# Performance work log

Measured on AMD Instinct MI355X. Metric: run time of the kernel, lower is better.

Reference implementation:

```python
import jax, jax.numpy as jnp
import numpy as np

B, Q, DIM, HEADS, RPE_H, HGRID, WGRID, STRIDE = 2, 900, 256, 8, 512, 64, 64, 16
KV = HGRID * WGRID


def setup_inputs() -> dict:
    key = jax.random.key(0)
    ks = jax.random.split(key, 16)
    s = 0.02
    return {
        "hidden_states": jax.random.normal(ks[0], (B, Q, DIM), jnp.float32),
        "reference_points": jax.random.uniform(ks[1], (B, Q, 1, 4), jnp.float32),
        "key_value_states": jax.random.normal(ks[2], (B, KV, DIM), jnp.float32),
        "spatial_shapes": jnp.array([[HGRID, WGRID]], dtype=jnp.int64),
        "attention_mask": jax.random.randint(ks[3], (B, KV), 0, 2, jnp.int32),
        "mlp1_w1": jax.random.normal(ks[4], (RPE_H, 2), jnp.float32) * s,
        "mlp1_b1": jnp.zeros((RPE_H,), jnp.float32),
        "mlp1_w2": jax.random.normal(ks[5], (HEADS, RPE_H), jnp.float32) * s,
        "mlp2_w1": jax.random.normal(ks[6], (RPE_H, 2), jnp.float32) * s,
        "mlp2_b1": jnp.zeros((RPE_H,), jnp.float32),
        "mlp2_w2": jax.random.normal(ks[7], (HEADS, RPE_H), jnp.float32) * s,
        "q_w": jax.random.normal(ks[8], (DIM, DIM), jnp.float32) * s,
        "q_b": jnp.zeros((DIM,), jnp.float32),
        "k_w": jax.random.normal(ks[9], (DIM, DIM), jnp.float32) * s,
        "k_b": jnp.zeros((DIM,), jnp.float32),
        "v_w": jax.random.normal(ks[10], (DIM, DIM), jnp.float32) * s,
        "v_b": jnp.zeros((DIM,), jnp.float32),
        "o_w": jax.random.normal(ks[11], (DIM, DIM), jnp.float32) * s,
        "o_b": jnp.zeros((DIM,), jnp.float32),
    }


def _attn(hidden_states, reference_points, key_value_states, h, w, attention_mask,
          mlp1_w1, mlp1_b1, mlp1_w2, mlp2_w1, mlp2_b1, mlp2_w2,
          q_w, q_b, k_w, k_b, v_w, v_b, o_w, o_b):
    b, q_len, dim = hidden_states.shape
    nh = mlp1_w2.shape[0]
    hd = dim // nh
    scale = hd ** -0.5
    stride = STRIDE

    # boxes cxcywh -> x1y1x2y2, scaled to absolute pixel coords (reparam=False)
    c, sz = reference_points[..., :2], reference_points[..., 2:]
    ref = jnp.concatenate([c - sz / 2, c + sz / 2], axis=-1)  # (B,Q,1,4)
    mult = jnp.array([w * stride, h * stride, w * stride, h * stride], dtype=ref.dtype)
    ref = ref * mult

    pos_x = (jnp.arange(w, dtype=jnp.float32) + 0.5) * stride
    pos_y = (jnp.arange(h, dtype=jnp.float32) + 0.5) * stride
    dx = ref[..., 0::2] - pos_x[None, None, :, None]  # (B,Q,W,2)
    dy = ref[..., 1::2] - pos_y[None, None, :, None]  # (B,Q,H,2)

    # small MLPs: 2 -> rpe_hidden -> num_heads
    rpe_x = jax.nn.relu(dx @ mlp1_w1.T + mlp1_b1) @ mlp1_w2.T  # (B,Q,W,nh)
    rpe_y = jax.nn.relu(dy @ mlp2_w1.T + mlp2_b1) @ mlp2_w2.T  # (B,Q,H,nh)
    rpe = rpe_x[:, :, None, :, :] + rpe_y[:, :, :, None, :]    # (B,Q,H,W,nh)
    rpe = rpe.reshape(b, q_len, h * w, nh).transpose(0, 3, 1, 2)  # (B,nh,Q,K)

    queries = (hidden_states @ q_w.T + q_b).reshape(b, q_len, nh, hd).transpose(0, 2, 1, 3) * scale
    kv_len = key_value_states.shape[1]
    keys = (key_value_states @ k_w.T + k_b).reshape(b, kv_len, nh, hd).transpose(0, 2, 1, 3)
    values = (key_value_states @ v_w.T + v_b).reshape(b, kv_len, nh, hd).transpose(0, 2, 1, 3)

    scores = jnp.einsum('bhqd,bhkd->bhqk', queries, keys) + rpe
    scores = scores + attention_mask.astype(scores.dtype)[:, None, None] * (-100.0)
    probs = jax.nn.softmax(scores, axis=-1)
    ctx = jnp.einsum('bhqk,bhkd->bhqd', probs, values)
    ctx = ctx.transpose(0, 2, 1, 3).reshape(b, q_len, dim)
    return ctx @ o_w.T + o_b


def reference(hidden_states, reference_points, key_value_states, spatial_shapes, attention_mask,
              mlp1_w1, mlp1_b1, mlp1_w2, mlp2_w1, mlp2_b1, mlp2_w2,
              q_w, q_b, k_w, k_b, v_w, v_b, o_w, o_b):
    h = int(spatial_shapes[0, 0])
    w = int(spatial_shapes[0, 1])
    return _attn(hidden_states, reference_points, key_value_states, h, w, attention_mask,
                 mlp1_w1, mlp1_b1, mlp1_w2, mlp2_w1, mlp2_b1, mlp2_w2,
                 q_w, q_b, k_w, k_b, v_w, v_b, o_w, o_b)
```

## Files before the change

### kernel.cpp

```cpp
#include <hip/hip_runtime.h>
#include <math.h>

#define NB    2
#define NQ    900
#define NQP   960
#define NKV   4096
#define DIMM  256
#define NHEAD 8
#define HD    32
#define RPEH  512
#define GRID  64
#define SPLIT 4

#define LOG2E 1.4426950408889634f

typedef short short8 __attribute__((ext_vector_type(8)));
typedef float f32x4 __attribute__((ext_vector_type(4)));
typedef unsigned uint2v __attribute__((ext_vector_type(2)));
typedef unsigned short u16;
typedef unsigned short u16x4 __attribute__((ext_vector_type(4)));

__device__ inline u16 f2bf(float f) {
    unsigned u = __builtin_bit_cast(unsigned, f);
    u += 0x7fff + ((u >> 16) & 1);
    return (u16)(u >> 16);
}
__device__ inline unsigned cvtpk_bf16(float a, float b) {
    unsigned r;
    asm("v_cvt_pk_bf16_f32 %0, %1, %2" : "=v"(r) : "v"(a), "v"(b));
    return r;
}

#define HS4  115200
#define KV4  524288
#define W4   16384
__global__ __launch_bounds__(256) void conv_bf16(
    const float* __restrict__ hs, const float* __restrict__ kv,
    const float* __restrict__ qw, const float* __restrict__ kw,
    const float* __restrict__ vw,
    u16* __restrict__ hsbf, u16* __restrict__ kvbf,
    u16* __restrict__ qwbf, u16* __restrict__ kwbf, u16* __restrict__ vwbf)
{
    const int total = HS4 + KV4 + 3 * W4;
    for (int g = blockIdx.x * 256 + threadIdx.x; g < total; g += gridDim.x * 256) {
        const float* s; u16* d; int off;
        if (g < HS4)                       { s = hs; d = hsbf; off = g; }
        else if (g < HS4 + KV4)            { s = kv; d = kvbf; off = g - HS4; }
        else if (g < HS4 + KV4 + W4)       { s = qw; d = qwbf; off = g - HS4 - KV4; }
        else if (g < HS4 + KV4 + 2 * W4)   { s = kw; d = kwbf; off = g - HS4 - KV4 - W4; }
        else                               { s = vw; d = vwbf; off = g - HS4 - KV4 - 2 * W4; }
        f32x4 v = *(const f32x4*)(s + (size_t)off * 4);
        *(u16x4*)(d + (size_t)off * 4) =
            (u16x4){f2bf(v[0]), f2bf(v[1]), f2bf(v[2]), f2bf(v[3])};
    }
}

__global__ __launch_bounds__(256) void proj_mfma(
    const u16* __restrict__ A,
    const u16* __restrict__ W0, const float* __restrict__ B0,
    const u16* __restrict__ W1, const float* __restrict__ B1,
    u16* __restrict__ outRow, u16* __restrict__ outVt,
    int M, float scale)
{
    __shared__ u16 Abuf[2][4096];
    __shared__ u16 Bbuf[2][4096];

    const u16* W = W0; const float* bias = B0; bool vt = false;
    if (blockIdx.z == 1) { W = W1; bias = B1; vt = true; }

    const int t    = threadIdx.x;
    const int lane = t & 63;
    const int w    = t >> 6;
    const int wm   = w >> 1, wn = w & 1;
    const int m0   = blockIdx.x * 128;
    const int n0   = blockIdx.y * 128;

    const int r0 = t >> 2, c0 = t & 3;
    const int r1 = r0 + 64;
    const int s0 = r0 * 4 + (c0 ^ (r0 & 3));
    const int s1 = r1 * 4 + (c0 ^ (r1 & 3));
    const u16* Arow0 = A + (size_t)(m0 + r0) * DIMM + c0 * 8;
    const u16* Arow1 = A + (size_t)(m0 + r1) * DIMM + c0 * 8;
    const u16* Wrow0 = W + (size_t)(n0 + r0) * DIMM + c0 * 8;
    const u16* Wrow1 = W + (size_t)(n0 + r1) * DIMM + c0 * 8;

    const int fr = lane & 15, fkc = lane >> 4;
    int aslot[4], bslot[4];
    #pragma unroll
    for (int f = 0; f < 4; ++f) {
        int ar = wm * 64 + f * 16 + fr;
        int br = wn * 64 + f * 16 + fr;
        aslot[f] = ar * 4 + (fkc ^ (ar & 3));
        bslot[f] = br * 4 + (fkc ^ (br & 3));
    }
    float bv[4];
    #pragma unroll
    for (int f = 0; f < 4; ++f) bv[f] = bias[n0 + wn * 64 + f * 16 + fr];

    f32x4 acc[4][4] = {};

    {
        short8 a0 = *(const short8*)(Arow0);
        short8 a1 = *(const short8*)(Arow1);
        short8 b0 = *(const short8*)(Wrow0);
        short8 b1 = *(const short8*)(Wrow1);
        *(short8*)&Abuf[0][s0 * 8] = a0;
        *(short8*)&Abuf[0][s1 * 8] = a1;
        *(short8*)&Bbuf[0][s0 * 8] = b0;
        *(short8*)&Bbuf[0][s1 * 8] = b1;
    }
    __syncthreads();

    int cur = 0;
    for (int kt = 0; kt < 8; ++kt) {
        short8 na0, na1, nb0, nb1;
        if (kt < 7) {
            int ko = (kt + 1) * 32;
            na0 = *(const short8*)(Arow0 + ko);
            na1 = *(const short8*)(Arow1 + ko);
            nb0 = *(const short8*)(Wrow0 + ko);
            nb1 = *(const short8*)(Wrow1 + ko);
        }
        short8 af[4], bf[4];
        #pragma unroll
        for (int f = 0; f < 4; ++f) {
            af[f] = *(const short8*)&Abuf[cur][aslot[f] * 8];
            bf[f] = *(const short8*)&Bbuf[cur][bslot[f] * 8];
        }
        #pragma unroll
        for (int i = 0; i < 4; ++i)
            #pragma unroll
            for (int j = 0; j < 4; ++j)
                acc[i][j] = __builtin_amdgcn_mfma_f32_16x16x32_bf16(af[i], bf[j], acc[i][j], 0, 0, 0);
        if (kt < 7) {
            *(short8*)&Abuf[cur ^ 1][s0 * 8] = na0;
            *(short8*)&Abuf[cur ^ 1][s1 * 8] = na1;
            *(short8*)&Bbuf[cur ^ 1][s0 * 8] = nb0;
            *(short8*)&Bbuf[cur ^ 1][s1 * 8] = nb1;
        }
        __syncthreads();
        cur ^= 1;
    }

    #pragma unroll
    for (int i = 0; i < 4; ++i) {
        int mbase = m0 + wm * 64 + i * 16 + 4 * fkc;
        #pragma unroll
        for (int j = 0; j < 4; ++j) {
            int n = n0 + wn * 64 + j * 16 + fr;
            #pragma unroll
            for (int r = 0; r < 4; ++r) {
                int gm = mbase + r;
                if (gm < M) {
                    float v = (acc[i][j][r] + bv[j]) * scale;
                    if (!vt) {
                        outRow[(size_t)gm * DIMM + n] = f2bf(v);
                    } else {
                        int bb = gm >> 12, kvi = gm & 4095;
                        int hh = n >> 5, dd = n & 31;
                        outVt[(size_t)((bb * NHEAD + hh) * HD + dd) * NKV + kvi] = f2bf(v);
                    }
                }
            }
        }
    }
}

__global__ __launch_bounds__(256) void rpe_kernel(
    const float* __restrict__ ref_pts,
    const float* __restrict__ w1x, const float* __restrict__ b1x,
    const float* __restrict__ w2x,
    const float* __restrict__ w1y, const float* __restrict__ b1y,
    const float* __restrict__ w2y,
    float* __restrict__ rpex, float* __restrict__ rpey)
{
    __shared__ f32x4 wpk[RPEH];
    __shared__ float w2t[RPEH][NHEAD];
    __shared__ float2 red[3][4][4][64];

    const int t   = threadIdx.x;
    const int m   = blockIdx.x & 1;
    const int bq0 = (blockIdx.x >> 1) * 4;

    const float* w1 = m ? w1y : w1x;
    const float* b1 = m ? b1y : b1x;
    const float* w2 = m ? w2y : w2x;
    for (int r = t; r < RPEH; r += 256) {
        float a = w1[r * 2], b = w1[r * 2 + 1];
        wpk[r] = (f32x4){a, b, b1[r], a + b};
    }
    for (int i = t; i < RPEH * NHEAD; i += 256) {
        int h = i >> 9, r = i & 511;
        w2t[r][h] = w2[h * RPEH + r] * LOG2E;
    }
    __syncthreads();

    const int lane = t & 63;
    const int wv   = t >> 6;
    const float p  = (lane + 0.5f) * 16.f;

    float lo[4], hi[4];
    #pragma unroll
    for (int j = 0; j < 4; ++j) {
        const float* q = ref_pts + (size_t)(bq0 + j) * 4;
        float c = m ? q[1] : q[0];
        float s = m ? q[3] : q[2];
        lo[j] = (c - s * 0.5f) * 1024.f;
        hi[j] = (c + s * 0.5f) * 1024.f;
    }

    float2 acc[4][4] = {};
    const int r0 = wv * 128;
    #pragma unroll 4
    for (int rr = 0; rr < 128; ++rr) {
        int r = r0 + rr;
        f32x4 W  = wpk[r];
        f32x4 u0 = *(const f32x4*)&w2t[r][0];
        f32x4 u1 = *(const f32x4*)&w2t[r][4];
        float bp = W[3] * p;
        #pragma unroll
        for (int tk = 0; tk < 4; ++tk) {
            float al  = W[0] * lo[tk] + W[1] * hi[tk] + W[2];
            float hid = fmaxf(al - bp, 0.f);
            acc[tk][0].x += u0[0] * hid;  acc[tk][0].y += u0[1] * hid;
            acc[tk][1].x += u0[2] * hid;  acc[tk][1].y += u0[3] * hid;
            acc[tk][2].x += u1[0] * hid;  acc[tk][2].y += u1[1] * hid;
            acc[tk][3].x += u1[2] * hid;  acc[tk][3].y += u1[3] * hid;
        }
    }

    if (wv > 0) {
        #pragma unroll
        for (int tk = 0; tk < 4; ++tk)
            #pragma unroll
            for (int j = 0; j < 4; ++j)
                red[wv - 1][tk][j][lane] = acc[tk][j];
    }
    __syncthreads();
    if (wv == 0) {
        float* outp = m ? rpey : rpex;
        #pragma unroll
        for (int tk = 0; tk < 4; ++tk) {
            size_t base = (size_t)(bq0 + tk) * (NHEAD * GRID) + lane;
            #pragma unroll
            for (int j = 0; j < 4; ++j) {
                float2 s0 = red[0][tk][j][lane];
                float2 s1 = red[1][tk][j][lane];
                float2 s2 = red[2][tk][j][lane];
                float sx = acc[tk][j].x + s0.x + s1.x + s2.x;
                float sy = acc[tk][j].y + s0.y + s1.y + s2.y;
                outp[base + (2 * j) * GRID]     = sx;
                outp[base + (2 * j + 1) * GRID] = sy;
            }
        }
    }
}

__global__ __launch_bounds__(256) void attn_mfma(
    const u16* __restrict__ Qbf, const u16* __restrict__ Kbf,
    const u16* __restrict__ Vt,
    const float* __restrict__ RX, const float* __restrict__ RY,
    const int* __restrict__ mask,
    float* __restrict__ pctx, float2* __restrict__ pml)
{
    constexpr int KSEG = NKV / SPLIT;
    constexpr int NTS  = KSEG / 64;
    __shared__ short8 kbuf[2][4][64];
    __shared__ short8 vbuf[2][4][64];
    __shared__ unsigned pbuf[4][64][4];
    __shared__ float ry_s[NTS][68];
    __shared__ float mbuf[2][64];

    const int tid  = threadIdx.x;
    const int lane = tid & 63;
    const int w    = tid >> 6;
    const int q15  = lane & 15;
    const int g    = lane >> 4;
    const int qt = blockIdx.x, h = blockIdx.y;
    const int b  = blockIdx.z / SPLIT;
    const int sp = blockIdx.z % SPLIT;
    const int q0 = qt * 64;
    const int wq = w * 16 + q15;
    const int gq = q0 + wq;
    const bool qok = gq < NQ;
    const int kv0g = sp * KSEG;

    float rxr[16];
    {
        const float* rxrow = RX + (size_t)(b * NQ + (qok ? gq : 0)) * (NHEAD * GRID) + h * GRID;
        #pragma unroll
        for (int kt = 0; kt < 4; ++kt)
            #pragma unroll
            for (int r = 0; r < 4; ++r)
                rxr[kt * 4 + r] = qok ? rxrow[16 * kt + 4 * g + r] : 0.f;
    }
    for (int idx = tid; idx < NTS * 64; idx += 256) {
        int y = idx & (NTS - 1), q = idx / NTS;
        int gq2 = q0 + q;
        ry_s[y][q] = (gq2 < NQ)
            ? RY[(size_t)(b * NQ + gq2) * (NHEAD * GRID) + h * GRID + sp * NTS + y] : 0.f;
    }

    short8 qf = *(const short8*)(Qbf + ((size_t)(b * NQ + gq)) * DIMM + h * HD + 8 * g);

    const int sr = tid >> 2, sc = tid & 3;
    const int vd = tid >> 3, vc = tid & 7;
    const size_t kbase = ((size_t)(b * NKV + kv0g + sr)) * DIMM + h * HD + 8 * sc;
    const size_t vbase = ((size_t)((b * NHEAD + h) * HD + vd)) * NKV + kv0g + 8 * vc;

    kbuf[0][sr >> 4][(sr & 15) + 16 * sc] = *(const short8*)(Kbf + kbase);
    vbuf[0][(vc >> 2) * 2 + (vd >> 4)][16 * (vc & 3) + (vd & 15)] = *(const short8*)(Vt + vbase);
    if (tid < 64) mbuf[0][tid] = -(100.f * LOG2E) * (float)mask[b * NKV + kv0g + tid];
    __syncthreads();

    f32x4 cacc0 = {0.f, 0.f, 0.f, 0.f};
    f32x4 cacc1 = {0.f, 0.f, 0.f, 0.f};
    float m_run = -1e30f, l_run = 0.f;
    int cur = 0;

    for (int t = 0; t < NTS; ++t) {
        short8 rk = {}, rv = {};
        float rm = 0.f;
        if (t < NTS - 1) {
            size_t kvn = (size_t)(t + 1) * 64;
            rk = *(const short8*)(Kbf + kbase + kvn * DIMM);
            rv = *(const short8*)(Vt + vbase + kvn);
            if (tid < 64) rm = -(100.f * LOG2E) * (float)mask[b * NKV + kv0g + kvn + tid];
        }

        f32x4 zero = {0.f, 0.f, 0.f, 0.f};
        f32x4 s[4];
        __builtin_amdgcn_s_setprio(1);
        #pragma unroll
        for (int kt = 0; kt < 4; ++kt)
            s[kt] = __builtin_amdgcn_mfma_f32_16x16x32_bf16(kbuf[cur][kt][lane], qf, zero, 0, 0, 0);
        __builtin_amdgcn_s_setprio(0);

        float ryb = ry_s[t][wq];
        #pragma unroll
        for (int kt = 0; kt < 4; ++kt) {
            #pragma unroll
            for (int r = 0; r < 4; ++r)
                s[kt][r] += rxr[kt * 4 + r] + ryb + mbuf[cur][16 * kt + 4 * g + r];
        }

        float mk[4];
        #pragma unroll
        for (int kt = 0; kt < 4; ++kt)
            mk[kt] = fmaxf(fmaxf(s[kt][0], s[kt][1]), fmaxf(s[kt][2], s[kt][3]));
        float mloc = fmaxf(fmaxf(mk[0], mk[1]), fmaxf(mk[2], mk[3]));
        mloc = fmaxf(mloc, __shfl_xor(mloc, 16));
        mloc = fmaxf(mloc, __shfl_xor(mloc, 32));

        if (!__all(mloc <= m_run + 8.f)) {
            float mnew = fmaxf(m_run, mloc);
            float fsc  = exp2f(m_run - mnew);
            l_run *= fsc;
            cacc0 *= fsc;
            cacc1 *= fsc;
            m_run = mnew;
        }

        float psum = 0.f;
        #pragma unroll
        for (int kt = 0; kt < 4; ++kt)
            #pragma unroll
            for (int r = 0; r < 4; ++r) {
                float pv = exp2f(s[kt][r] - m_run);
                s[kt][r] = pv;
                psum += pv;
            }
        psum += __shfl_xor(psum, 16);
        psum += __shfl_xor(psum, 32);
        l_run += psum;

        __builtin_amdgcn_s_setprio(1);
        #pragma unroll
        for (int sk = 0; sk < 2; ++sk) {
            #pragma unroll
            for (int kk = 0; kk < 2; ++kk) {
                int kt = sk * 2 + kk;
                unsigned d0 = cvtpk_bf16(s[kt][0], s[kt][1]);
                unsigned d1 = cvtpk_bf16(s[kt][2], s[kt][3]);
                int lt = 16 * ((2 * kt + (g >> 1)) & 3) + q15;
                uint2v* dst = (uint2v*)&pbuf[w][lt][2 * (g & 1)];
                *dst = (uint2v){d0, d1};
            }
            short8 pf = *(const short8*)&pbuf[w][lane][0];
            cacc0 = __builtin_amdgcn_mfma_f32_16x16x32_bf16(vbuf[cur][sk * 2 + 0][lane], pf, cacc0, 0, 0, 0);
            cacc1 = __builtin_amdgcn_mfma_f32_16x16x32_bf16(vbuf[cur][sk * 2 + 1][lane], pf, cacc1, 0, 0, 0);
        }
        __builtin_amdgcn_s_setprio(0);

        if (t < NTS - 1) {
            kbuf[cur ^ 1][sr >> 4][(sr & 15) + 16 * sc] = rk;
            vbuf[cur ^ 1][(vc >> 2) * 2 + (vd >> 4)][16 * (vc & 3) + (vd & 15)] = rv;
            if (tid < 64) mbuf[cur ^ 1][tid] = rm;
        }
        __syncthreads();
        cur ^= 1;
    }

    size_t prow = (size_t)(sp * NB + b) * NQP + gq;
    float* pc = pctx + prow * DIMM + h * HD;
    #pragma unroll
    for (int r = 0; r < 4; ++r) {
        pc[4 * g + r]      = cacc0[r];
        pc[16 + 4 * g + r] = cacc1[r];
    }
    if (g == 0) {
        float2 v; v.x = m_run; v.y = l_run;
        pml[prow * NHEAD + h] = v;
    }
}

__global__ __launch_bounds__(256) void attn_reduce(
    const float* __restrict__ pctx, const float2* __restrict__ pml,
    float* __restrict__ CTX)
{
    const int bq = blockIdx.x;
    const int b = bq / NQ, q = bq - b * NQ;
    const int c = threadIdx.x;
    const int h = c >> 5;

    float m[SPLIT], l[SPLIT];
    #pragma unroll
    for (int sp = 0; sp < SPLIT; ++sp) {
        float2 v = pml[((size_t)(sp * NB + b) * NQP + q) * NHEAD + h];
        m[sp] = v.x; l[sp] = v.y;
    }
    float ms = fmaxf(fmaxf(m[0], m[1]), fmaxf(m[2], m[3]));
    float L = 0.f, acc = 0.f;
    #pragma unroll
    for (int sp = 0; sp < SPLIT; ++sp) {
        float wgt = exp2f(m[sp] - ms);
        L   += wgt * l[sp];
        acc += wgt * pctx[((size_t)(sp * NB + b) * NQP + q) * DIMM + c];
    }
    CTX[(size_t)bq * DIMM + c] = acc / L;
}

__global__ __launch_bounds__(256) void gemm_bias_f32(
    const float* __restrict__ A, const float* __restrict__ W,
    const float* __restrict__ bias, float* __restrict__ C,
    int M, int N, int K)
{
    __shared__ float As[32][33];
    __shared__ float Ws[32][33];
    const int t  = threadIdx.x;
    const int tr = t >> 4;
    const int tc = t & 15;
    const int brow = blockIdx.y * 32;
    const int bcol = blockIdx.x * 32;
    float acc00 = 0.f, acc01 = 0.f, acc10 = 0.f, acc11 = 0.f;

    for (int kt = 0; kt < K; kt += 32) {
        #pragma unroll
        for (int i = 0; i < 4; ++i) {
            int idx = t + i * 256;
            int r = idx >> 5, c = idx & 31;
            int gr = brow + r;
            As[r][c] = (gr < M) ? A[(size_t)gr * K + kt + c] : 0.f;
            Ws[r][c] = W[(size_t)(bcol + r) * K + kt + c];
        }
        __syncthreads();
        #pragma unroll 8
        for (int k = 0; k < 32; ++k) {
            float a0 = As[tr * 2][k], a1 = As[tr * 2 + 1][k];
            float w0 = Ws[tc * 2][k], w1 = Ws[tc * 2 + 1][k];
            acc00 += a0 * w0; acc01 += a0 * w1;
            acc10 += a1 * w0; acc11 += a1 * w1;
        }
        __syncthreads();
    }
    int gc0 = bcol + tc * 2, gc1 = gc0 + 1;
    int gr0 = brow + tr * 2, gr1 = gr0 + 1;
    if (gr0 < M) {
        C[(size_t)gr0 * N + gc0] = acc00 + bias[gc0];
        C[(size_t)gr0 * N + gc1] = acc01 + bias[gc1];
    }
    if (gr1 < M) {
        C[(size_t)gr1 * N + gc0] = acc10 + bias[gc0];
        C[(size_t)gr1 * N + gc1] = acc11 + bias[gc1];
    }
}

extern "C" void kernel_launch(void* const* d_in, const int* in_sizes, int n_in,
                              void* d_out, int out_size, void* d_ws, size_t ws_size,
                              hipStream_t stream)
{
    const float* hs   = (const float*)d_in[0];
    const float* rp   = (const float*)d_in[1];
    const float* kv   = (const float*)d_in[2];
    const int*   msk  = (const int*)d_in[4];
    const float* m1w1 = (const float*)d_in[5];
    const float* m1b1 = (const float*)d_in[6];
    const float* m1w2 = (const float*)d_in[7];
    const float* m2w1 = (const float*)d_in[8];
    const float* m2b1 = (const float*)d_in[9];
    const float* m2w2 = (const float*)d_in[10];
    const float* q_w  = (const float*)d_in[11];
    const float* q_b  = (const float*)d_in[12];
    const float* k_w  = (const float*)d_in[13];
    const float* k_b  = (const float*)d_in[14];
    const float* v_w  = (const float*)d_in[15];
    const float* v_b  = (const float*)d_in[16];
    const float* o_w  = (const float*)d_in[17];
    const float* o_b  = (const float*)d_in[18];
    float* out = (float*)d_out;

    char* p = (char*)d_ws;
    float* RX   = (float*)p; p += (size_t)NB * NQ * NHEAD * GRID * 4;
    float* RY   = (float*)p; p += (size_t)NB * NQ * NHEAD * GRID * 4;
    float* CTX  = (float*)p; p += (size_t)NB * NQ * DIMM * 4;
    u16*   Qbf  = (u16*)p;   p += (size_t)1920 * DIMM * 2;
    u16*   Kbf  = (u16*)p;   p += (size_t)NB * NKV * DIMM * 2;
    u16*   Vt   = (u16*)p;   p += (size_t)NB * NHEAD * HD * NKV * 2;

    char* u = p;
    u16* hsbf = (u16*)u;
    u16* kvbf = hsbf + (size_t)1920 * DIMM;
    u16* qwbf = kvbf + (size_t)NB * NKV * DIMM;
    u16* kwbf = qwbf + (size_t)DIMM * DIMM;
    u16* vwbf = kwbf + (size_t)DIMM * DIMM;
    float*  pctx = (float*)u;
    float2* pml  = (float2*)(pctx + (size_t)SPLIT * NB * NQP * DIMM);

    const float scale = 0.17677669529663687f * LOG2E;

    conv_bf16<<<1024, 256, 0, stream>>>(hs, kv, q_w, k_w, v_w,
                                        hsbf, kvbf, qwbf, kwbf, vwbf);

    proj_mfma<<<dim3(15, 2, 1), 256, 0, stream>>>(
        hsbf, qwbf, q_b, nullptr, nullptr, Qbf, nullptr, NB * NQ, scale);

    proj_mfma<<<dim3(64, 2, 2), 256, 0, stream>>>(
        kvbf, kwbf, k_b, vwbf, v_b, Kbf, Vt, NB * NKV, 1.f);

    rpe_kernel<<<900, 256, 0, stream>>>(rp, m1w1, m1b1, m1w2,
                                        m2w1, m2b1, m2w2, RX, RY);

    attn_mfma<<<dim3((NQ + 63) / 64, NHEAD, NB * SPLIT), 256, 0, stream>>>(
        Qbf, Kbf, Vt, RX, RY, msk, pctx, pml);

    attn_reduce<<<NB * NQ, 256, 0, stream>>>(pctx, pml, CTX);

    gemm_bias_f32<<<dim3(DIMM / 32, (NB * NQ + 31) / 32), 256, 0, stream>>>(
        CTX, o_w, o_b, out, NB * NQ, DIMM, DIMM);
}
```

Before: 141.6 us.

## Load K/V fragments directly from global memory, drop LDS staging and barriers

Removes the shared-memory double buffers for K, V, mask and RY in the attention kernel. Each wave now loads its MFMA operand fragments straight from global memory (relying on L1/L2 reuse across the four waves), which eliminates the per-tile __syncthreads. The mask is pre-converted to scaled floats in the conversion kernel so the attention loop can read it as vectors. The trade-off is four times more global/L2 traffic per block and no explicit prefetch, so global latency is exposed unless the compiler or other waves hide it.

```diff
diff --git a/kernel.cpp b/kernel.cpp
--- a/kernel.cpp
+++ b/kernel.cpp
@@ -17,6 +17,7 @@
 typedef short short8 __attribute__((ext_vector_type(8)));
 typedef float f32x4 __attribute__((ext_vector_type(4)));
 typedef unsigned uint2v __attribute__((ext_vector_type(2)));
+typedef int int4v __attribute__((ext_vector_type(4)));
 typedef unsigned short u16;
 typedef unsigned short u16x4 __attribute__((ext_vector_type(4)));
 
@@ -34,15 +35,25 @@
 #define HS4  115200
 #define KV4  524288
 #define W4   16384
+#define M4   2048
 __global__ __launch_bounds__(256) void conv_bf16(
     const float* __restrict__ hs, const float* __restrict__ kv,
     const float* __restrict__ qw, const float* __restrict__ kw,
-    const float* __restrict__ vw,
+    const float* __restrict__ vw, const int* __restrict__ msk,
     u16* __restrict__ hsbf, u16* __restrict__ kvbf,
-    u16* __restrict__ qwbf, u16* __restrict__ kwbf, u16* __restrict__ vwbf)
-{
-    const int total = HS4 + KV4 + 3 * W4;
+    u16* __restrict__ qwbf, u16* __restrict__ kwbf, u16* __restrict__ vwbf,
+    float* __restrict__ Mb)
+{
+    const int total = HS4 + KV4 + 3 * W4 + M4;
     for (int g = blockIdx.x * 256 + threadIdx.x; g < total; g += gridDim.x * 256) {
+        if (g >= HS4 + KV4 + 3 * W4) {
+            int off = g - (HS4 + KV4 + 3 * W4);
+            int4v m = *(const int4v*)(msk + (size_t)off * 4);
+            f32x4 o = {-(100.f * LOG2E) * (float)m[0], -(100.f * LOG2E) * (float)m[1],
+                       -(100.f * LOG2E) * (float)m[2], -(100.f * LOG2E) * (float)m[3]};
+            *(f32x4*)(Mb + (size_t)off * 4) = o;
+            continue;
+        }
         const float* s; u16* d; int off;
         if (g < HS4)                       { s = hs; d = hsbf; off = g; }
         else if (g < HS4 + KV4)            { s = kv; d = kvbf; off = g - HS4; }
@@ -260,16 +271,12 @@
     const u16* __restrict__ Qbf, const u16* __restrict__ Kbf,
     const u16* __restrict__ Vt,
     const float* __restrict__ RX, const float* __restrict__ RY,
-    const int* __restrict__ mask,
+    const float* __restrict__ Mb,
     float* __restrict__ pctx, float2* __restrict__ pml)
 {
     constexpr int KSEG = NKV / SPLIT;
     constexpr int NTS  = KSEG / 64;
-    __shared__ short8 kbuf[2][4][64];
-    __shared__ short8 vbuf[2][4][64];
     __shared__ unsigned pbuf[4][64][4];
-    __shared__ float ry_s[NTS][68];
-    __shared__ float mbuf[2][64];
 
     const int tid  = threadIdx.x;
     const int lane = tid & 63;
@@ -294,54 +301,47 @@
             for (int r = 0; r < 4; ++r)
                 rxr[kt * 4 + r] = qok ? rxrow[16 * kt + 4 * g + r] : 0.f;
     }
-    for (int idx = tid; idx < NTS * 64; idx += 256) {
-        int y = idx & (NTS - 1), q = idx / NTS;
-        int gq2 = q0 + q;
-        ry_s[y][q] = (gq2 < NQ)
-            ? RY[(size_t)(b * NQ + gq2) * (NHEAD * GRID) + h * GRID + sp * NTS + y] : 0.f;
-    }
+    const float* yrow = RY + (size_t)(b * NQ + (qok ? gq : 0)) * (NHEAD * GRID) + h * GRID + sp * NTS;
 
     short8 qf = *(const short8*)(Qbf + ((size_t)(b * NQ + gq)) * DIMM + h * HD + 8 * g);
 
-    const int sr = tid >> 2, sc = tid & 3;
-    const int vd = tid >> 3, vc = tid & 7;
-    const size_t kbase = ((size_t)(b * NKV + kv0g + sr)) * DIMM + h * HD + 8 * sc;
-    const size_t vbase = ((size_t)((b * NHEAD + h) * HD + vd)) * NKV + kv0g + 8 * vc;
-
-    kbuf[0][sr >> 4][(sr & 15) + 16 * sc] = *(const short8*)(Kbf + kbase);
-    vbuf[0][(vc >> 2) * 2 + (vd >> 4)][16 * (vc & 3) + (vd & 15)] = *(const short8*)(Vt + vbase);
-    if (tid < 64) mbuf[0][tid] = -(100.f * LOG2E) * (float)mask[b * NKV + kv0g + tid];
-    __syncthreads();
+    const u16* kb = Kbf + ((size_t)(b * NKV + kv0g + q15)) * DIMM + h * HD + 8 * g;
+    const u16* vb = Vt + ((size_t)((b * NHEAD + h) * HD + q15)) * NKV + kv0g + 8 * g;
+    const float* mb = Mb + (size_t)b * NKV + kv0g + 4 * g;
 
     f32x4 cacc0 = {0.f, 0.f, 0.f, 0.f};
     f32x4 cacc1 = {0.f, 0.f, 0.f, 0.f};
     float m_run = -1e30f, l_run = 0.f;
-    int cur = 0;
 
     for (int t = 0; t < NTS; ++t) {
-        short8 rk = {}, rv = {};
-        float rm = 0.f;
-        if (t < NTS - 1) {
-            size_t kvn = (size_t)(t + 1) * 64;
-            rk = *(const short8*)(Kbf + kbase + kvn * DIMM);
-            rv = *(const short8*)(Vt + vbase + kvn);
-            if (tid < 64) rm = -(100.f * LOG2E) * (float)mask[b * NKV + kv0g + kvn + tid];
-        }
+        short8 rk[4], rv[4];
+        f32x4 rm[4];
+        #pragma unroll
+        for (int kt = 0; kt < 4; ++kt)
+            rk[kt] = *(const short8*)(kb + (size_t)(64 * t + 16 * kt) * DIMM);
+        #pragma unroll
+        for (int sk = 0; sk < 2; ++sk)
+            #pragma unroll
+            for (int dt = 0; dt < 2; ++dt)
+                rv[sk * 2 + dt] = *(const short8*)(vb + (size_t)dt * 16 * NKV + 64 * t + 32 * sk);
+        #pragma unroll
+        for (int kt = 0; kt < 4; ++kt)
+            rm[kt] = *(const f32x4*)(mb + 64 * t + 16 * kt);
+        float ryb = qok ? yrow[t] : 0.f;
 
         f32x4 zero = {0.f, 0.f, 0.f, 0.f};
         f32x4 s[4];
         __builtin_amdgcn_s_setprio(1);
         #pragma unroll
         for (int kt = 0; kt < 4; ++kt)
-            s[kt] = __builtin_amdgcn_mfma_f32_16x16x32_bf16(kbuf[cur][kt][lane], qf, zero, 0, 0, 0);
+            s[kt] = __builtin_amdgcn_mfma_f32_16x16x32_bf16(rk[kt], qf, zero, 0, 0, 0);
         __builtin_amdgcn_s_setprio(0);
 
-        float ryb = ry_s[t][wq];
         #pragma unroll
         for (int kt = 0; kt < 4; ++kt) {
             #pragma unroll
             for (int r = 0; r < 4; ++r)
-                s[kt][r] += rxr[kt * 4 + r] + ryb + mbuf[cur][16 * kt + 4 * g + r];
+                s[kt][r] += rxr[kt * 4 + r] + ryb + rm[kt][r];
         }
 
         float mk[4];
@@ -387,18 +387,10 @@
                 *dst = (uint2v){d0, d1};
             }
             short8 pf = *(const short8*)&pbuf[w][lane][0];
-            cacc0 = __builtin_amdgcn_mfma_f32_16x16x32_bf16(vbuf[cur][sk * 2 + 0][lane], pf, cacc0, 0, 0, 0);
-            cacc1 = __builtin_amdgcn_mfma_f32_16x16x32_bf16(vbuf[cur][sk * 2 + 1][lane], pf, cacc1, 0, 0, 0);
+            cacc0 = __builtin_amdgcn_mfma_f32_16x16x32_bf16(rv[sk * 2 + 0], pf, cacc0, 0, 0, 0);
+            cacc1 = __builtin_amdgcn_mfma_f32_16x16x32_bf16(rv[sk * 2 + 1], pf, cacc1, 0, 0, 0);
         }
         __builtin_amdgcn_s_setprio(0);
-
-        if (t < NTS - 1) {
-            kbuf[cur ^ 1][sr >> 4][(sr & 15) + 16 * sc] = rk;
-            vbuf[cur ^ 1][(vc >> 2) * 2 + (vd >> 4)][16 * (vc & 3) + (vd & 15)] = rv;
-            if (tid < 64) mbuf[cur ^ 1][tid] = rm;
-        }
-        __syncthreads();
-        cur ^= 1;
     }
 
     size_t prow = (size_t)(sp * NB + b) * NQP + gq;
@@ -516,6 +508,7 @@
     u16*   Qbf  = (u16*)p;   p += (size_t)1920 * DIMM * 2;
     u16*   Kbf  = (u16*)p;   p += (size_t)NB * NKV * DIMM * 2;
     u16*   Vt   = (u16*)p;   p += (size_t)NB * NHEAD * HD * NKV * 2;
+    float* Mb   = (float*)p; p += (size_t)NB * NKV * 4;
 
     char* u = p;
     u16* hsbf = (u16*)u;
@@ -528,8 +521,8 @@
 
     const float scale = 0.17677669529663687f * LOG2E;
 
-    conv_bf16<<<1024, 256, 0, stream>>>(hs, kv, q_w, k_w, v_w,
-                                        hsbf, kvbf, qwbf, kwbf, vwbf);
+    conv_bf16<<<1024, 256, 0, stream>>>(hs, kv, q_w, k_w, v_w, msk,
+                                        hsbf, kvbf, qwbf, kwbf, vwbf, Mb);
 
     proj_mfma<<<dim3(15, 2, 1), 256, 0, stream>>>(
         hsbf, qwbf, q_b, nullptr, nullptr, Qbf, nullptr, NB * NQ, scale);
@@ -541,7 +534,7 @@
                                         m2w1, m2b1, m2w2, RX, RY);
 
     attn_mfma<<<dim3((NQ + 63) / 64, NHEAD, NB * SPLIT), 256, 0, stream>>>(
-        Qbf, Kbf, Vt, RX, RY, msk, pctx, pml);
+        Qbf, Kbf, Vt, RX, RY, Mb, pctx, pml);
 
     attn_reduce<<<NB * NQ, 256, 0, stream>>>(pctx, pml, CTX);
 
```

New measurement: 178.1 us. 1.26x slower.

## Merge bf16 conversion with RPE kernel and fuse Q/K/V projections into one launch

Applied to the files above, without the earlier changes.

The bf16 conversion and the RPE MLP now run as one prep kernel, with blocks split by index between the two jobs, so the small-grid RPE work overlaps the bandwidth-bound conversion. The Q projection and the K/V projections are merged into a single proj_mfma launch using blockIdx.z=2 for Q, with excess blocks exiting early. This drops two kernel launches and their serialization gaps, but the prep kernel now always reserves the RPE shared memory, which may lower occupancy for the conversion blocks.

```diff
diff --git a/kernel.cpp b/kernel.cpp
--- a/kernel.cpp
+++ b/kernel.cpp
@@ -34,39 +34,139 @@
 #define HS4  115200
 #define KV4  524288
 #define W4   16384
-__global__ __launch_bounds__(256) void conv_bf16(
+#define CONVB 1024
+__global__ __launch_bounds__(256) void prep_kernel(
     const float* __restrict__ hs, const float* __restrict__ kv,
     const float* __restrict__ qw, const float* __restrict__ kw,
     const float* __restrict__ vw,
+    const float* __restrict__ ref_pts,
+    const float* __restrict__ w1x, const float* __restrict__ b1x,
+    const float* __restrict__ w2x,
+    const float* __restrict__ w1y, const float* __restrict__ b1y,
+    const float* __restrict__ w2y,
     u16* __restrict__ hsbf, u16* __restrict__ kvbf,
-    u16* __restrict__ qwbf, u16* __restrict__ kwbf, u16* __restrict__ vwbf)
+    u16* __restrict__ qwbf, u16* __restrict__ kwbf, u16* __restrict__ vwbf,
+    float* __restrict__ rpex, float* __restrict__ rpey)
 {
-    const int total = HS4 + KV4 + 3 * W4;
-    for (int g = blockIdx.x * 256 + threadIdx.x; g < total; g += gridDim.x * 256) {
-        const float* s; u16* d; int off;
-        if (g < HS4)                       { s = hs; d = hsbf; off = g; }
-        else if (g < HS4 + KV4)            { s = kv; d = kvbf; off = g - HS4; }
-        else if (g < HS4 + KV4 + W4)       { s = qw; d = qwbf; off = g - HS4 - KV4; }
-        else if (g < HS4 + KV4 + 2 * W4)   { s = kw; d = kwbf; off = g - HS4 - KV4 - W4; }
-        else                               { s = vw; d = vwbf; off = g - HS4 - KV4 - 2 * W4; }
-        f32x4 v = *(const f32x4*)(s + (size_t)off * 4);
-        *(u16x4*)(d + (size_t)off * 4) =
-            (u16x4){f2bf(v[0]), f2bf(v[1]), f2bf(v[2]), f2bf(v[3])};
+    __shared__ f32x4 wpk[RPEH];
+    __shared__ float w2t[RPEH][NHEAD];
+    __shared__ float2 red[3][4][4][64];
+
+    const int t = threadIdx.x;
+
+    if (blockIdx.x < CONVB) {
+        const int total = HS4 + KV4 + 3 * W4;
+        for (int g = blockIdx.x * 256 + t; g < total; g += CONVB * 256) {
+            const float* s; u16* d; int off;
+            if (g < HS4)                       { s = hs; d = hsbf; off = g; }
+            else if (g < HS4 + KV4)            { s = kv; d = kvbf; off = g - HS4; }
+            else if (g < HS4 + KV4 + W4)       { s = qw; d = qwbf; off = g - HS4 - KV4; }
+            else if (g < HS4 + KV4 + 2 * W4)   { s = kw; d = kwbf; off = g - HS4 - KV4 - W4; }
+            else                               { s = vw; d = vwbf; off = g - HS4 - KV4 - 2 * W4; }
+            f32x4 v = *(const f32x4*)(s + (size_t)off * 4);
+            *(u16x4*)(d + (size_t)off * 4) =
+                (u16x4){f2bf(v[0]), f2bf(v[1]), f2bf(v[2]), f2bf(v[3])};
+        }
+        return;
+    }
+
+    const int bid = blockIdx.x - CONVB;
+    const int m   = bid & 1;
+    const int bq0 = (bid >> 1) * 4;
+
+    const float* w1 = m ? w1y : w1x;
+    const float* b1 = m ? b1y : b1x;
+    const float* w2 = m ? w2y : w2x;
+    for (int r = t; r < RPEH; r += 256) {
+        float a = w1[r * 2], b = w1[r * 2 + 1];
+        wpk[r] = (f32x4){a, b, b1[r], a + b};
+    }
+    for (int i = t; i < RPEH * NHEAD; i += 256) {
+        int h = i >> 9, r = i & 511;
+        w2t[r][h] = w2[h * RPEH + r] * LOG2E;
+    }
+    __syncthreads();
+
+    const int lane = t & 63;
+    const int wv   = t >> 6;
+    const float p  = (lane + 0.5f) * 16.f;
+
+    float lo[4], hi[4];
+    #pragma unroll
+    for (int j = 0; j < 4; ++j) {
+        const float* q = ref_pts + (size_t)(bq0 + j) * 4;
+        float c = m ? q[1] : q[0];
+        float s = m ? q[3] : q[2];
+        lo[j] = (c - s * 0.5f) * 1024.f;
+        hi[j] = (c + s * 0.5f) * 1024.f;
+    }
+
+    float2 acc[4][4] = {};
+    const int r0 = wv * 128;
+    #pragma unroll 4
+    for (int rr = 0; rr < 128; ++rr) {
+        int r = r0 + rr;
+        f32x4 W  = wpk[r];
+        f32x4 u0 = *(const f32x4*)&w2t[r][0];
+        f32x4 u1 = *(const f32x4*)&w2t[r][4];
+        float bp = W[3] * p;
+        #pragma unroll
+        for (int tk = 0; tk < 4; ++tk) {
+            float al  = W[0] * lo[tk] + W[1] * hi[tk] + W[2];
+            float hid = fmaxf(al - bp, 0.f);
+            acc[tk][0].x += u0[0] * hid;  acc[tk][0].y += u0[1] * hid;
+            acc[tk][1].x += u0[2] * hid;  acc[tk][1].y += u0[3] * hid;
+            acc[tk][2].x += u1[0] * hid;  acc[tk][2].y += u1[1] * hid;
+            acc[tk][3].x += u1[2] * hid;  acc[tk][3].y += u1[3] * hid;
+        }
+    }
+
+    if (wv > 0) {
+        #pragma unroll
+        for (int tk = 0; tk < 4; ++tk)
+            #pragma unroll
+            for (int j = 0; j < 4; ++j)
+                red[wv - 1][tk][j][lane] = acc[tk][j];
+    }
+    __syncthreads();
+    if (wv == 0) {
+        float* outp = m ? rpey : rpex;
+        #pragma unroll
+        for (int tk = 0; tk < 4; ++tk) {
+            size_t base = (size_t)(bq0 + tk) * (NHEAD * GRID) + lane;
+            #pragma unroll
+            for (int j = 0; j < 4; ++j) {
+                float2 s0 = red[0][tk][j][lane];
+                float2 s1 = red[1][tk][j][lane];
+                float2 s2 = red[2][tk][j][lane];
+                float sx = acc[tk][j].x + s0.x + s1.x + s2.x;
+                float sy = acc[tk][j].y + s0.y + s1.y + s2.y;
+                outp[base + (2 * j) * GRID]     = sx;
+                outp[base + (2 * j + 1) * GRID] = sy;
+            }
+        }
     }
 }
 
 __global__ __launch_bounds__(256) void proj_mfma(
-    const u16* __restrict__ A,
-    const u16* __restrict__ W0, const float* __restrict__ B0,
-    const u16* __restrict__ W1, const float* __restrict__ B1,
-    u16* __restrict__ outRow, u16* __restrict__ outVt,
-    int M, float scale)
+    const u16* __restrict__ hsbf, const u16* __restrict__ kvbf,
+    const u16* __restrict__ qwbf, const float* __restrict__ q_b,
+    const u16* __restrict__ kwbf, const float* __restrict__ k_b,
+    const u16* __restrict__ vwbf, const float* __restrict__ v_b,
+    u16* __restrict__ Qbf, u16* __restrict__ Kbf, u16* __restrict__ Vt,
+    float scaleQ)
 {
     __shared__ u16 Abuf[2][4096];
     __shared__ u16 Bbuf[2][4096];
 
-    const u16* W = W0; const float* bias = B0; bool vt = false;
-    if (blockIdx.z == 1) { W = W1; bias = B1; vt = true; }
+    const u16* A; const u16* W; const float* bias;
+    u16* outRow = nullptr; bool vt = false; int M; float scale = 1.f;
+    if (blockIdx.z == 0)      { A = kvbf; W = kwbf; bias = k_b; outRow = Kbf; M = NB * NKV; }
+    else if (blockIdx.z == 1) { A = kvbf; W = vwbf; bias = v_b; vt = true;   M = NB * NKV; }
+    else {
+        if (blockIdx.x >= 15) return;
+        A = hsbf; W = qwbf; bias = q_b; outRow = Qbf; M = NB * NQ; scale = scaleQ;
+    }
 
     const int t    = threadIdx.x;
     const int lane = t & 63;
@@ -158,99 +258,9 @@
                     } else {
                         int bb = gm >> 12, kvi = gm & 4095;
                         int hh = n >> 5, dd = n & 31;
-                        outVt[(size_t)((bb * NHEAD + hh) * HD + dd) * NKV + kvi] = f2bf(v);
+                        Vt[(size_t)((bb * NHEAD + hh) * HD + dd) * NKV + kvi] = f2bf(v);
                     }
                 }
-            }
-        }
-    }
-}
-
-__global__ __launch_bounds__(256) void rpe_kernel(
-    const float* __restrict__ ref_pts,
-    const float* __restrict__ w1x, const float* __restrict__ b1x,
-    const float* __restrict__ w2x,
-    const float* __restrict__ w1y, const float* __restrict__ b1y,
-    const float* __restrict__ w2y,
-    float* __restrict__ rpex, float* __restrict__ rpey)
-{
-    __shared__ f32x4 wpk[RPEH];
-    __shared__ float w2t[RPEH][NHEAD];
-    __shared__ float2 red[3][4][4][64];
-
-    const int t   = threadIdx.x;
-    const int m   = blockIdx.x & 1;
-    const int bq0 = (blockIdx.x >> 1) * 4;
-
-    const float* w1 = m ? w1y : w1x;
-    const float* b1 = m ? b1y : b1x;
-    const float* w2 = m ? w2y : w2x;
-    for (int r = t; r < RPEH; r += 256) {
-        float a = w1[r * 2], b = w1[r * 2 + 1];
-        wpk[r] = (f32x4){a, b, b1[r], a + b};
-    }
-    for (int i = t; i < RPEH * NHEAD; i += 256) {
-        int h = i >> 9, r = i & 511;
-        w2t[r][h] = w2[h * RPEH + r] * LOG2E;
-    }
-    __syncthreads();
-
-    const int lane = t & 63;
-    const int wv   = t >> 6;
-    const float p  = (lane + 0.5f) * 16.f;
-
-    float lo[4], hi[4];
-    #pragma unroll
-    for (int j = 0; j < 4; ++j) {
-        const float* q = ref_pts + (size_t)(bq0 + j) * 4;
-        float c = m ? q[1] : q[0];
-        float s = m ? q[3] : q[2];
-        lo[j] = (c - s * 0.5f) * 1024.f;
-        hi[j] = (c + s * 0.5f) * 1024.f;
-    }
-
-    float2 acc[4][4] = {};
-    const int r0 = wv * 128;
-    #pragma unroll 4
-    for (int rr = 0; rr < 128; ++rr) {
-        int r = r0 + rr;
-        f32x4 W  = wpk[r];
-        f32x4 u0 = *(const f32x4*)&w2t[r][0];
-        f32x4 u1 = *(const f32x4*)&w2t[r][4];
-        float bp = W[3] * p;
-        #pragma unroll
-        for (int tk = 0; tk < 4; ++tk) {
-            float al  = W[0] * lo[tk] + W[1] * hi[tk] + W[2];
-            float hid = fmaxf(al - bp, 0.f);
-            acc[tk][0].x += u0[0] * hid;  acc[tk][0].y += u0[1] * hid;
-            acc[tk][1].x += u0[2] * hid;  acc[tk][1].y += u0[3] * hid;
-            acc[tk][2].x += u1[0] * hid;  acc[tk][2].y += u1[1] * hid;
-            acc[tk][3].x += u1[2] * hid;  acc[tk][3].y += u1[3] * hid;
-        }
-    }
-
-    if (wv > 0) {
-        #pragma unroll
-        for (int tk = 0; tk < 4; ++tk)
-            #pragma unroll
-            for (int j = 0; j < 4; ++j)
-                red[wv - 1][tk][j][lane] = acc[tk][j];
-    }
-    __syncthreads();
-    if (wv == 0) {
-        float* outp = m ? rpey : rpex;
-        #pragma unroll
-        for (int tk = 0; tk < 4; ++tk) {
-            size_t base = (size_t)(bq0 + tk) * (NHEAD * GRID) + lane;
-            #pragma unroll
-            for (int j = 0; j < 4; ++j) {
-                float2 s0 = red[0][tk][j][lane];
-                float2 s1 = red[1][tk][j][lane];
-                float2 s2 = red[2][tk][j][lane];
-                float sx = acc[tk][j].x + s0.x + s1.x + s2.x;
-                float sy = acc[tk][j].y + s0.y + s1.y + s2.y;
-                outp[base + (2 * j) * GRID]     = sx;
-                outp[base + (2 * j + 1) * GRID] = sy;
             }
         }
     }
@@ -528,17 +538,12 @@
 
     const float scale = 0.17677669529663687f * LOG2E;
 
-    conv_bf16<<<1024, 256, 0, stream>>>(hs, kv, q_w, k_w, v_w,
-                                        hsbf, kvbf, qwbf, kwbf, vwbf);
-
-    proj_mfma<<<dim3(15, 2, 1), 256, 0, stream>>>(
-        hsbf, qwbf, q_b, nullptr, nullptr, Qbf, nullptr, NB * NQ, scale);
-
-    proj_mfma<<<dim3(64, 2, 2), 256, 0, stream>>>(
-        kvbf, kwbf, k_b, vwbf, v_b, Kbf, Vt, NB * NKV, 1.f);
-
-    rpe_kernel<<<900, 256, 0, stream>>>(rp, m1w1, m1b1, m1w2,
-                                        m2w1, m2b1, m2w2, RX, RY);
+    prep_kernel<<<CONVB + 900, 256, 0, stream>>>(
+        hs, kv, q_w, k_w, v_w, rp, m1w1, m1b1, m1w2, m2w1, m2b1, m2w2,
+        hsbf, kvbf, qwbf, kwbf, vwbf, RX, RY);
+
+    proj_mfma<<<dim3(64, 2, 3), 256, 0, stream>>>(
+        hsbf, kvbf, qwbf, q_b, kwbf, k_b, vwbf, v_b, Qbf, Kbf, Vt, scale);
 
     attn_mfma<<<dim3((NQ + 63) / 64, NHEAD, NB * SPLIT), 256, 0, stream>>>(
         Qbf, Kbf, Vt, RX, RY, msk, pctx, pml);
```

Measured after the change: 129.3 us (median of 3 runs). 1.09x faster.
